# Kernel optimization log

Hardware: AMD Instinct MI355X
Metric: run time of the kernel (lower is better)

The kernel has to match this reference:

```python
import jax, jax.numpy as jnp
import numpy as np

TOP_K = 8
ROUTED_SCALING = 2.5


def setup_inputs() -> dict:
    key = jax.random.key(0)
    ks = jax.random.split(key, 8)
    B, S, H, E, I = 2, 1024, 2048, 32, 1024
    IS = 2 * I  # shared expert intermediate (n_shared_experts * moe_intermediate_size)
    w = lambda k, shape: jax.random.normal(k, shape, dtype=jnp.float32) * 0.02
    return {
        "hidden_states": jax.random.normal(ks[0], (B, S, H), dtype=jnp.float32),
        "gate_weight": w(ks[1], (E, H)),
        "w_gate": w(ks[2], (E, H, I)),
        "w_up": w(ks[3], (E, H, I)),
        "w_down": w(ks[4], (E, I, H)),
        "ws_gate": w(ks[5], (H, IS)),
        "ws_up": w(ks[6], (H, IS)),
        "ws_down": w(ks[7], (IS, H)),
    }


def reference(hidden_states, gate_weight, w_gate, w_up, w_down, ws_gate, ws_up, ws_down):
    B, S, H = hidden_states.shape
    x = hidden_states.reshape(-1, H)  # [T, H]
    T = x.shape[0]
    E = gate_weight.shape[0]

    # --- gate (DeepseekV3 top-k router: sigmoid scores, top-k, renormalize, scale) ---
    scores = jax.nn.sigmoid(x @ gate_weight.T)              # [T, E]
    topk_w, topk_i = jax.lax.top_k(scores, TOP_K)           # [T, K]
    topk_w = topk_w / (jnp.sum(topk_w, axis=-1, keepdims=True) + 1e-20)
    topk_w = topk_w * ROUTED_SCALING

    # dense [T, E] combine weights (scatter of top-k weights; zeros elsewhere)
    dense_w = jnp.zeros((T, E), dtype=topk_w.dtype).at[
        jnp.arange(T)[:, None], topk_i
    ].add(topk_w)

    # --- all experts on all tokens (calibrate_all_experts semantics; non-selected get weight 0) ---
    g = jnp.einsum('th,ehi->eti', x, w_gate)                # [E, T, I]
    u = jnp.einsum('th,ehi->eti', x, w_up)                  # [E, T, I]
    eo = jnp.einsum('eti,eih->eth', jax.nn.silu(g) * u, w_down)  # [E, T, H]
    routed = jnp.einsum('eth,te->th', eo, dense_w)          # weighted scatter-combine

    # --- shared expert (gated SiLU MLP on residual) ---
    shared = (jax.nn.silu(x @ ws_gate) * (x @ ws_up)) @ ws_down

    return (routed + shared).reshape(B, S, H)
```

## Files before the change

kernel.cpp:

```cpp
#include <hip/hip_runtime.h>

#define T_TOK 2048
#define H_DIM 2048
#define E_NUM 32
#define I_DIM 1024
#define IS_DIM 2048
#define K_TOT (E_NUM * I_DIM + IS_DIM)
#define SLOT_CAP 2048
#define MAX_TILES 160

typedef __bf16 bf16x8 __attribute__((ext_vector_type(8)));
typedef float  f32x4  __attribute__((ext_vector_type(4)));
static_assert(sizeof(bf16x8) == 16, "bf16x8 must be 16B");

#define OFF_CNT   ((size_t)0)
#define OFF_NT    ((size_t)128)
#define OFF_TILES ((size_t)256)
#define OFF_PAIRS ((size_t)1024)
#define OFF_XB    ((size_t)263168)
#define OFF_WGT   ((size_t)8651776)
#define OFF_WUT   ((size_t)142869504)
#define OFF_HS    OFF_WUT
#define OFF_WSGT  ((size_t)277087232)
#define OFF_WSUT  ((size_t)285475840)
#define OFF_WDT   ((size_t)293864448)
#define OFF_ACT   ((size_t)436470784)

__device__ __forceinline__ unsigned short f2bf(float f) {
  unsigned int u = __float_as_uint(f);
  u += 0x7fffu + ((u >> 16) & 1u);
  return (unsigned short)(u >> 16);
}

__device__ __forceinline__ void gld16(const void* g, void* l) {
  __builtin_amdgcn_global_load_lds(
      (const __attribute__((address_space(1))) unsigned int*)g,
      (__attribute__((address_space(3))) unsigned int*)l, 16, 0, 0);
}

__global__ __launch_bounds__(256) void router_kernel(
    const float* __restrict__ x, const float* __restrict__ gw,
    int* __restrict__ cnt, unsigned int* __restrict__ pairs)
{
  const int t = blockIdx.x;
  __shared__ float xs[H_DIM];
  __shared__ float sc[E_NUM];
  const float4* xr = (const float4*)(x + (long)t * H_DIM);
  for (int i = threadIdx.x; i < H_DIM / 4; i += 256) ((float4*)xs)[i] = xr[i];
  __syncthreads();
  const int e = threadIdx.x >> 3, p = threadIdx.x & 7;
  const float4* ga = (const float4*)(gw + (long)e * H_DIM);
  const float4* xa = (const float4*)xs;
  float s = 0.f;
  #pragma unroll 4
  for (int i = p * 64; i < p * 64 + 64; ++i) {
    float4 a = ga[i], b = xa[i];
    s += a.x * b.x + a.y * b.y + a.z * b.z + a.w * b.w;
  }
  s += __shfl_down(s, 4, 8);
  s += __shfl_down(s, 2, 8);
  s += __shfl_down(s, 1, 8);
  if (p == 0) sc[e] = 1.f / (1.f + expf(-s));
  __syncthreads();
  if (threadIdx.x == 0) {
    float v[E_NUM];
    #pragma unroll
    for (int i = 0; i < E_NUM; ++i) v[i] = sc[i];
    unsigned mask = 0; float sum = 0.f;
    int sel[8]; float wv[8];
    for (int k = 0; k < 8; ++k) {
      float best = -1.f; int bi = 0;
      for (int i = 0; i < E_NUM; ++i)
        if (!((mask >> i) & 1u) && v[i] > best) { best = v[i]; bi = i; }
      mask |= 1u << bi; sel[k] = bi; wv[k] = best; sum += best;
    }
    const float scale = 2.5f / (sum + 1e-20f);
    for (int k = 0; k < 8; ++k) {
      const int slot = atomicAdd(&cnt[sel[k]], 1);
      if (slot < SLOT_CAP) {
        const unsigned int w16 = (unsigned int)f2bf(wv[k] * scale);
        pairs[sel[k] * SLOT_CAP + slot] = (w16 << 16) | (unsigned int)t;
      }
    }
  }
}

__global__ void build_tiles_kernel(const int* __restrict__ cnt,
                                   unsigned int* __restrict__ tiles,
                                   int* __restrict__ ntp)
{
  if (threadIdx.x == 0 && blockIdx.x == 0) {
    int n = 0;
    for (int e = 0; e < E_NUM; ++e) {
      const int c = cnt[e];
      for (int m0 = 0; m0 < c; m0 += 128)
        tiles[n++] = ((unsigned int)e << 16) | (unsigned int)m0;
    }
    *ntp = n;
  }
}

__global__ __launch_bounds__(256) void cvt_bf16_kernel(
    const float* __restrict__ in, unsigned short* __restrict__ out, int n4)
{
  int i = blockIdx.x * 256 + threadIdx.x;
  if (i >= n4) return;
  float4 v = ((const float4*)in)[i];
  ushort4 o;
  o.x = f2bf(v.x); o.y = f2bf(v.y); o.z = f2bf(v.z); o.w = f2bf(v.w);
  ((ushort4*)out)[i] = o;
}

struct TDescTable {
  const float* in[6];
  unsigned short* out[6];
  int C[6];
  int ldout[6];
  long in_bs[6];
  long out_bs[6];
  int nbx[6];
  int nbxy[6];
  int start[7];
};

__global__ __launch_bounds__(256) void transpose_fused(TDescTable td)
{
  const int bid = blockIdx.x;
  int i = 0;
  while (i < 5 && bid >= td.start[i + 1]) ++i;
  const int local = bid - td.start[i];
  const int bz = local / td.nbxy[i];
  const int rem = local % td.nbxy[i];
  const int by = rem / td.nbx[i];
  const int bx = rem % td.nbx[i];
  const float* in = td.in[i] + (long)bz * td.in_bs[i];
  unsigned short* out = td.out[i] + (long)bz * td.out_bs[i];
  const int C = td.C[i], ldout = td.ldout[i];

  __shared__ float tile[64][65];
  const int c0 = bx * 64;
  const int r0 = by * 64;
  const int t = threadIdx.x;
  const int lr = t >> 4;
  const int lc = (t & 15) << 2;
  #pragma unroll
  for (int rr = 0; rr < 64; rr += 16) {
    float4 v = *(const float4*)(in + (long)(r0 + lr + rr) * C + c0 + lc);
    tile[lr + rr][lc + 0] = v.x;
    tile[lr + rr][lc + 1] = v.y;
    tile[lr + rr][lc + 2] = v.z;
    tile[lr + rr][lc + 3] = v.w;
  }
  __syncthreads();
  #pragma unroll
  for (int rr = 0; rr < 64; rr += 16) {
    const int c = c0 + lr + rr;
    ushort4 o;
    o.x = f2bf(tile[lc + 0][lr + rr]);
    o.y = f2bf(tile[lc + 1][lr + rr]);
    o.z = f2bf(tile[lc + 2][lr + rr]);
    o.w = f2bf(tile[lc + 3][lr + rr]);
    *(ushort4*)(out + (long)c * ldout + r0 + lc) = o;
  }
}

__global__ __launch_bounds__(512, 4) void gate_up_moe_kernel(
    const unsigned short* __restrict__ xb,
    const unsigned short* __restrict__ bgT,
    const unsigned short* __restrict__ buT,
    const int* __restrict__ cnt,
    const unsigned int* __restrict__ pairs,
    const unsigned int* __restrict__ tiles,
    const int* __restrict__ ntp,
    unsigned short* __restrict__ act)
{
  const int ti = blockIdx.y;
  if (ti >= *ntp) return;
  const unsigned int tile = tiles[ti];
  const int e  = (int)(tile >> 16);
  const int m0 = (int)(tile & 0xFFFFu);
  const int cnte = cnt[e];
  const int n0 = blockIdx.x * 64;
  const unsigned short* Bg = bgT + ((long)e * I_DIM + n0) * H_DIM;
  const unsigned short* Bu = buT + ((long)e * I_DIM + n0) * H_DIM;

  __shared__ unsigned short sA[2][128 * 64];
  __shared__ unsigned short sBg[2][64 * 64];
  __shared__ unsigned short sBu[2][64 * 64];

  const int tid = threadIdx.x;
  const int lane = tid & 63;
  const int wid = tid >> 6;
  const int wm = wid >> 1, wn = wid & 1;
  const int l15 = lane & 15;
  const int lk  = (lane >> 4) * 8;
  const int srow = tid >> 3;
  const int scol = (tid & 7) * 8;
  const int scolsw = (((tid & 7) ^ (srow & 7))) * 8;
  const int ksw = (l15 & 7) << 3;

  const unsigned short* asrc[2];
  #pragma unroll
  for (int r = 0; r < 2; ++r) {
    const int slot = m0 + r * 64 + srow;
    const unsigned int pr = (slot < cnte) ? pairs[e * SLOT_CAP + slot] : 0u;
    asrc[r] = xb + (long)(pr & 0xFFFFu) * H_DIM + scolsw;
  }

  const f32x4 fz = {0.f, 0.f, 0.f, 0.f};
  f32x4 accg[2][2], accu[2][2];
  #pragma unroll
  for (int i = 0; i < 2; ++i)
    #pragma unroll
    for (int j = 0; j < 2; ++j) { accg[i][j] = fz; accu[i][j] = fz; }

#define STAGE_GU(buf, k0) do {                                                 \
    gld16(asrc[0] + (k0), sA[buf] + srow * 64 + scol);                         \
    gld16(asrc[1] + (k0), sA[buf] + (64 + srow) * 64 + scol);                  \
    gld16(Bg + (long)srow * H_DIM + (k0) + scolsw,                             \
          sBg[buf] + srow * 64 + scol);                                        \
    gld16(Bu + (long)srow * H_DIM + (k0) + scolsw,                             \
          sBu[buf] + srow * 64 + scol);                                        \
  } while (0)

#define COMP_GU(buf) do {                                                      \
    _Pragma("unroll")                                                          \
    for (int kk = 0; kk < 2; ++kk) {                                           \
      const int ko = kk * 32 + lk;                                             \
      bf16x8 a[2], g[2], u[2];                                                 \
      _Pragma("unroll")                                                        \
      for (int mi = 0; mi < 2; ++mi)                                           \
        a[mi] = *(const bf16x8*)(sA[buf] + (wm * 32 + mi * 16 + l15) * 64 +    \
                                 (ko ^ ksw));                                  \
      _Pragma("unroll")                                                        \
      for (int ni = 0; ni < 2; ++ni) {                                         \
        g[ni] = *(const bf16x8*)(sBg[buf] + (wn * 32 + ni * 16 + l15) * 64 +   \
                                 (ko ^ ksw));                                  \
        u[ni] = *(const bf16x8*)(sBu[buf] + (wn * 32 + ni * 16 + l15) * 64 +   \
                                 (ko ^ ksw));                                  \
      }                                                                        \
      _Pragma("unroll")                                                        \
      for (int mi = 0; mi < 2; ++mi)                                           \
        _Pragma("unroll")                                                      \
        for (int ni = 0; ni < 2; ++ni) {                                       \
          accg[mi][ni] = __builtin_amdgcn_mfma_f32_16x16x32_bf16(              \
              a[mi], g[ni], accg[mi][ni], 0, 0, 0);                            \
          accu[mi][ni] = __builtin_amdgcn_mfma_f32_16x16x32_bf16(              \
              a[mi], u[ni], accu[mi][ni], 0, 0, 0);                            \
        }                                                                      \
    }                                                                          \
  } while (0)

  STAGE_GU(0, 0);
  __syncthreads();
  for (int t = 0; t < 32; t += 2) {
    if (t + 1 < 32) STAGE_GU(1, (t + 1) * 64);
    COMP_GU(0);
    __syncthreads();
    if (t + 2 < 32) STAGE_GU(0, (t + 2) * 64);
    COMP_GU(1);
    __syncthreads();
  }
#undef STAGE_GU
#undef COMP_GU

  const int colb = n0 + wn * 32;
  #pragma unroll
  for (int mi = 0; mi < 2; ++mi) {
    #pragma unroll
    for (int r = 0; r < 4; ++r) {
      const int slot = m0 + wm * 32 + mi * 16 + (lane >> 4) * 4 + r;
      if (slot < cnte) {
        const unsigned int pr = pairs[e * SLOT_CAP + slot];
        const float w = __uint_as_float(pr & 0xFFFF0000u);
        #pragma unroll
        for (int ni = 0; ni < 2; ++ni) {
          const float gv = accg[mi][ni][r];
          const float uv = accu[mi][ni][r];
          const float sv = (gv / (1.f + expf(-gv))) * uv * w;
          act[((long)e * SLOT_CAP + slot) * I_DIM + colb + ni * 16 + l15] =
              f2bf(sv);
        }
      }
    }
  }
}

__global__ __launch_bounds__(256) void gate_up_shared_kernel(
    const unsigned short* __restrict__ xb,
    const unsigned short* __restrict__ bgT,
    const unsigned short* __restrict__ buT,
    unsigned short* __restrict__ hs)
{
  const int t0 = blockIdx.x * 128;
  const int n0 = blockIdx.y * 64;
  const unsigned short* Bg = bgT + (long)n0 * H_DIM;
  const unsigned short* Bu = buT + (long)n0 * H_DIM;
  const unsigned short* A  = xb + (long)t0 * H_DIM;

  __shared__ unsigned short sA[128 * 64];
  __shared__ unsigned short sBg[64 * 64];
  __shared__ unsigned short sBu[64 * 64];

  const int tid = threadIdx.x;
  const int lane = tid & 63;
  const int wid = tid >> 6;
  const int wm = wid >> 1, wn = wid & 1;
  const int l15 = lane & 15;
  const int lk  = (lane >> 4) * 8;
  const int srow = tid >> 3;
  const int scol = (tid & 7) * 8;
  const int scolsw = (((tid & 7) ^ ((tid >> 3) & 7))) * 8;
  const int ksw = (l15 & 7) << 3;

  const f32x4 fz = {0.f, 0.f, 0.f, 0.f};
  f32x4 accg[4][2], accu[4][2];
  #pragma unroll
  for (int i = 0; i < 4; ++i)
    #pragma unroll
    for (int j = 0; j < 2; ++j) { accg[i][j] = fz; accu[i][j] = fz; }

  for (int k0 = 0; k0 < H_DIM; k0 += 64) {
    #pragma unroll
    for (int r = 0; r < 4; ++r)
      gld16(A + (long)(r * 32 + srow) * H_DIM + k0 + scolsw,
            sA + (r * 32 + srow) * 64 + scol);
    #pragma unroll
    for (int r = 0; r < 2; ++r) {
      gld16(Bg + (long)(r * 32 + srow) * H_DIM + k0 + scolsw,
            sBg + (r * 32 + srow) * 64 + scol);
      gld16(Bu + (long)(r * 32 + srow) * H_DIM + k0 + scolsw,
            sBu + (r * 32 + srow) * 64 + scol);
    }
    __syncthreads();
    #pragma unroll
    for (int kk = 0; kk < 2; ++kk) {
      const int ko = kk * 32 + lk;
      bf16x8 a[4], g[2], u[2];
      #pragma unroll
      for (int mi = 0; mi < 4; ++mi)
        a[mi] = *(const bf16x8*)(sA + (wm * 64 + mi * 16 + l15) * 64 + (ko ^ ksw));
      #pragma unroll
      for (int ni = 0; ni < 2; ++ni) {
        g[ni] = *(const bf16x8*)(sBg + (wn * 32 + ni * 16 + l15) * 64 + (ko ^ ksw));
        u[ni] = *(const bf16x8*)(sBu + (wn * 32 + ni * 16 + l15) * 64 + (ko ^ ksw));
      }
      #pragma unroll
      for (int mi = 0; mi < 4; ++mi)
        #pragma unroll
        for (int ni = 0; ni < 2; ++ni) {
          accg[mi][ni] = __builtin_amdgcn_mfma_f32_16x16x32_bf16(a[mi], g[ni], accg[mi][ni], 0, 0, 0);
          accu[mi][ni] = __builtin_amdgcn_mfma_f32_16x16x32_bf16(a[mi], u[ni], accu[mi][ni], 0, 0, 0);
        }
    }
    __syncthreads();
  }

  const int colb = n0 + wn * 32;
  #pragma unroll
  for (int mi = 0; mi < 4; ++mi) {
    #pragma unroll
    for (int r = 0; r < 4; ++r) {
      const int t = t0 + wm * 64 + mi * 16 + (lane >> 4) * 4 + r;
      #pragma unroll
      for (int ni = 0; ni < 2; ++ni) {
        const float gv = accg[mi][ni][r];
        const float uv = accu[mi][ni][r];
        hs[(long)t * IS_DIM + colb + ni * 16 + l15] =
            f2bf((gv / (1.f + expf(-gv))) * uv);
      }
    }
  }
}

__global__ __launch_bounds__(256) void down_shared_kernel(
    const unsigned short* __restrict__ hs,
    const unsigned short* __restrict__ wdT,
    float* __restrict__ out)
{
  const int t0 = blockIdx.x * 128;
  const int n0 = blockIdx.y * 64;
  const unsigned short* A = hs + (long)t0 * IS_DIM;
  const unsigned short* B = wdT + (long)n0 * K_TOT;

  __shared__ unsigned short sA[128 * 64];
  __shared__ unsigned short sB[64 * 64];

  const int tid = threadIdx.x;
  const int lane = tid & 63;
  const int wid = tid >> 6;
  const int wm = wid >> 1, wn = wid & 1;
  const int l15 = lane & 15;
  const int lk  = (lane >> 4) * 8;
  const int srow = tid >> 3;
  const int scol = (tid & 7) * 8;
  const int scolsw = (((tid & 7) ^ ((tid >> 3) & 7))) * 8;
  const int ksw = (l15 & 7) << 3;

  const f32x4 fz = {0.f, 0.f, 0.f, 0.f};
  f32x4 acc[4][2];
  #pragma unroll
  for (int i = 0; i < 4; ++i)
    #pragma unroll
    for (int j = 0; j < 2; ++j) acc[i][j] = fz;

  for (int k0 = 0; k0 < IS_DIM; k0 += 64) {
    #pragma unroll
    for (int r = 0; r < 4; ++r)
      gld16(A + (long)(r * 32 + srow) * IS_DIM + k0 + scolsw,
            sA + (r * 32 + srow) * 64 + scol);
    #pragma unroll
    for (int r = 0; r < 2; ++r)
      gld16(B + (long)(r * 32 + srow) * K_TOT + k0 + scolsw,
            sB + (r * 32 + srow) * 64 + scol);
    __syncthreads();
    #pragma unroll
    for (int kk = 0; kk < 2; ++kk) {
      const int ko = kk * 32 + lk;
      bf16x8 a[4], b[2];
      #pragma unroll
      for (int mi = 0; mi < 4; ++mi)
        a[mi] = *(const bf16x8*)(sA + (wm * 64 + mi * 16 + l15) * 64 + (ko ^ ksw));
      #pragma unroll
      for (int ni = 0; ni < 2; ++ni)
        b[ni] = *(const bf16x8*)(sB + (wn * 32 + ni * 16 + l15) * 64 + (ko ^ ksw));
      #pragma unroll
      for (int mi = 0; mi < 4; ++mi)
        #pragma unroll
        for (int ni = 0; ni < 2; ++ni)
          acc[mi][ni] = __builtin_amdgcn_mfma_f32_16x16x32_bf16(a[mi], b[ni], acc[mi][ni], 0, 0, 0);
    }
    __syncthreads();
  }

  #pragma unroll
  for (int mi = 0; mi < 4; ++mi) {
    #pragma unroll
    for (int r = 0; r < 4; ++r) {
      const int t = t0 + wm * 64 + mi * 16 + (lane >> 4) * 4 + r;
      #pragma unroll
      for (int ni = 0; ni < 2; ++ni)
        out[(long)t * H_DIM + n0 + wn * 32 + ni * 16 + l15] = acc[mi][ni][r];
    }
  }
}

__global__ __launch_bounds__(512, 4) void down_moe_kernel(
    const unsigned short* __restrict__ act,
    const unsigned short* __restrict__ wdT,
    const int* __restrict__ cnt,
    const unsigned int* __restrict__ pairs,
    const unsigned int* __restrict__ tiles,
    const int* __restrict__ ntp,
    float* __restrict__ out)
{
  const int ti = blockIdx.y;
  if (ti >= *ntp) return;
  const unsigned int tile = tiles[ti];
  const int e  = (int)(tile >> 16);
  const int m0 = (int)(tile & 0xFFFFu);
  const int cnte = cnt[e];
  const int n0 = blockIdx.x * 64;
  const unsigned short* A = act + ((long)e * SLOT_CAP + m0) * I_DIM;
  const unsigned short* B = wdT + (long)n0 * K_TOT + (long)e * I_DIM;

  __shared__ unsigned short sA[2][128 * 64];
  __shared__ unsigned short sB[2][64 * 64];

  const int tid = threadIdx.x;
  const int lane = tid & 63;
  const int wid = tid >> 6;
  const int wm = wid >> 1, wn = wid & 1;
  const int l15 = lane & 15;
  const int lk  = (lane >> 4) * 8;
  const int srow = tid >> 3;
  const int scol = (tid & 7) * 8;
  const int scolsw = (((tid & 7) ^ (srow & 7))) * 8;
  const int ksw = (l15 & 7) << 3;

  const f32x4 fz = {0.f, 0.f, 0.f, 0.f};
  f32x4 acc[2][2];
  #pragma unroll
  for (int i = 0; i < 2; ++i)
    #pragma unroll
    for (int j = 0; j < 2; ++j) acc[i][j] = fz;

#define STAGE_DN(buf, k0) do {                                                 \
    gld16(A + (long)srow * I_DIM + (k0) + scolsw,                              \
          sA[buf] + srow * 64 + scol);                                         \
    gld16(A + (long)(64 + srow) * I_DIM + (k0) + scolsw,                       \
          sA[buf] + (64 + srow) * 64 + scol);                                  \
    gld16(B + (long)srow * K_TOT + (k0) + scolsw,                              \
          sB[buf] + srow * 64 + scol);                                         \
  } while (0)

#define COMP_DN(buf) do {                                                      \
    _Pragma("unroll")                                                          \
    for (int kk = 0; kk < 2; ++kk) {                                           \
      const int ko = kk * 32 + lk;                                             \
      bf16x8 a[2], b[2];                                                       \
      _Pragma("unroll")                                                        \
      for (int mi = 0; mi < 2; ++mi)                                           \
        a[mi] = *(const bf16x8*)(sA[buf] + (wm * 32 + mi * 16 + l15) * 64 +    \
                                 (ko ^ ksw));                                  \
      _Pragma("unroll")                                                        \
      for (int ni = 0; ni < 2; ++ni)                                           \
        b[ni] = *(const bf16x8*)(sB[buf] + (wn * 32 + ni * 16 + l15) * 64 +    \
                                 (ko ^ ksw));                                  \
      _Pragma("unroll")                                                        \
      for (int mi = 0; mi < 2; ++mi)                                           \
        _Pragma("unroll")                                                      \
        for (int ni = 0; ni < 2; ++ni)                                         \
          acc[mi][ni] = __builtin_amdgcn_mfma_f32_16x16x32_bf16(               \
              a[mi], b[ni], acc[mi][ni], 0, 0, 0);                             \
    }                                                                          \
  } while (0)

  STAGE_DN(0, 0);
  __syncthreads();
  for (int t = 0; t < 16; t += 2) {
    if (t + 1 < 16) STAGE_DN(1, (t + 1) * 64);
    COMP_DN(0);
    __syncthreads();
    if (t + 2 < 16) STAGE_DN(0, (t + 2) * 64);
    COMP_DN(1);
    __syncthreads();
  }
#undef STAGE_DN
#undef COMP_DN

  #pragma unroll
  for (int mi = 0; mi < 2; ++mi) {
    #pragma unroll
    for (int r = 0; r < 4; ++r) {
      const int slot = m0 + wm * 32 + mi * 16 + (lane >> 4) * 4 + r;
      if (slot < cnte) {
        const int tok = (int)(pairs[e * SLOT_CAP + slot] & 0xFFFFu);
        #pragma unroll
        for (int ni = 0; ni < 2; ++ni)
          atomicAdd(out + (long)tok * H_DIM + n0 + wn * 32 + ni * 16 + l15,
                    acc[mi][ni][r]);
      }
    }
  }
}

extern "C" void kernel_launch(void* const* d_in, const int* in_sizes, int n_in,
                              void* d_out, int out_size, void* d_ws, size_t ws_size,
                              hipStream_t stream) {
  (void)in_sizes; (void)n_in; (void)out_size; (void)ws_size;
  const float* x   = (const float*)d_in[0];
  const float* gw  = (const float*)d_in[1];
  const float* wg  = (const float*)d_in[2];
  const float* wu  = (const float*)d_in[3];
  const float* wd  = (const float*)d_in[4];
  const float* wsg = (const float*)d_in[5];
  const float* wsu = (const float*)d_in[6];
  const float* wsd = (const float*)d_in[7];
  float* out = (float*)d_out;
  char* ws = (char*)d_ws;

  int*            cnt   = (int*)(ws + OFF_CNT);
  int*            ntp   = (int*)(ws + OFF_NT);
  unsigned int*   tiles = (unsigned int*)(ws + OFF_TILES);
  unsigned int*   pairs = (unsigned int*)(ws + OFF_PAIRS);
  unsigned short* xb    = (unsigned short*)(ws + OFF_XB);
  unsigned short* wgT   = (unsigned short*)(ws + OFF_WGT);
  unsigned short* wuT   = (unsigned short*)(ws + OFF_WUT);
  unsigned short* hsb   = (unsigned short*)(ws + OFF_HS);
  unsigned short* wsgT  = (unsigned short*)(ws + OFF_WSGT);
  unsigned short* wsuT  = (unsigned short*)(ws + OFF_WSUT);
  unsigned short* wdT   = (unsigned short*)(ws + OFF_WDT);
  unsigned short* actb  = (unsigned short*)(ws + OFF_ACT);

  hipMemsetAsync(ws + OFF_CNT, 0, 128, stream);

  router_kernel<<<T_TOK, 256, 0, stream>>>(x, gw, cnt, pairs);
  build_tiles_kernel<<<1, 64, 0, stream>>>(cnt, tiles, ntp);
  cvt_bf16_kernel<<<(T_TOK * H_DIM / 4 + 255) / 256, 256, 0, stream>>>(
      x, xb, T_TOK * H_DIM / 4);

  TDescTable td;
  td.in[0] = wg;  td.out[0] = wgT;  td.C[0] = I_DIM;  td.ldout[0] = H_DIM;
  td.in_bs[0] = (long)H_DIM * I_DIM; td.out_bs[0] = (long)I_DIM * H_DIM;
  td.nbx[0] = I_DIM / 64; td.nbxy[0] = (I_DIM / 64) * (H_DIM / 64);
  td.in[1] = wu;  td.out[1] = wuT;  td.C[1] = I_DIM;  td.ldout[1] = H_DIM;
  td.in_bs[1] = (long)H_DIM * I_DIM; td.out_bs[1] = (long)I_DIM * H_DIM;
  td.nbx[1] = I_DIM / 64; td.nbxy[1] = (I_DIM / 64) * (H_DIM / 64);
  td.in[2] = wd;  td.out[2] = wdT;  td.C[2] = H_DIM;  td.ldout[2] = K_TOT;
  td.in_bs[2] = (long)I_DIM * H_DIM; td.out_bs[2] = (long)I_DIM;
  td.nbx[2] = H_DIM / 64; td.nbxy[2] = (H_DIM / 64) * (I_DIM / 64);
  td.in[3] = wsg; td.out[3] = wsgT; td.C[3] = IS_DIM; td.ldout[3] = H_DIM;
  td.in_bs[3] = 0; td.out_bs[3] = 0;
  td.nbx[3] = IS_DIM / 64; td.nbxy[3] = (IS_DIM / 64) * (H_DIM / 64);
  td.in[4] = wsu; td.out[4] = wsuT; td.C[4] = IS_DIM; td.ldout[4] = H_DIM;
  td.in_bs[4] = 0; td.out_bs[4] = 0;
  td.nbx[4] = IS_DIM / 64; td.nbxy[4] = (IS_DIM / 64) * (H_DIM / 64);
  td.in[5] = wsd; td.out[5] = wdT + E_NUM * I_DIM; td.C[5] = H_DIM;
  td.ldout[5] = K_TOT; td.in_bs[5] = 0; td.out_bs[5] = 0;
  td.nbx[5] = H_DIM / 64; td.nbxy[5] = (H_DIM / 64) * (IS_DIM / 64);
  td.start[0] = 0;
  for (int i = 0; i < 5; ++i) {
    int nz = (i <= 2) ? E_NUM : 1;
    td.start[i + 1] = td.start[i] + td.nbxy[i] * nz;
  }
  td.start[6] = td.start[5] + td.nbxy[5];
  transpose_fused<<<td.start[6], 256, 0, stream>>>(td);

  gate_up_moe_kernel<<<dim3(16, MAX_TILES), 512, 0, stream>>>(
      xb, wgT, wuT, cnt, pairs, tiles, ntp, actb);

  gate_up_shared_kernel<<<dim3(16, 32), 256, 0, stream>>>(
      xb, wsgT, wsuT, hsb);

  down_shared_kernel<<<dim3(16, 32), 256, 0, stream>>>(
      hsb, wdT + E_NUM * I_DIM, out);
  down_moe_kernel<<<dim3(32, MAX_TILES), 512, 0, stream>>>(
      actb, wdT, cnt, pairs, tiles, ntp, out);
}
```

Measured before the change: 865.8 us.

## Fold shared expert into grouped MoE GEMMs as pseudo-experts; widen transpose tiles

The shared expert is treated as two extra pseudo-experts (32, 33) with all tokens and weight 1.0. This lets the grouped gate/up and down kernels handle it, and the two separate shared-expert kernels are removed. Activations are packed compactly using per-expert base offsets. The down kernel runs 32 K-steps for the shared tile, with address remapping across the two halves. The transpose kernel now converts to bf16 before writing to LDS and uses 64x256 tiles with 16-byte stores. The output must be zeroed with a memset because everything now accumulates atomically, which adds atomic traffic for the shared part.

```diff
diff --git a/kernel.cpp b/kernel.cpp
--- a/kernel.cpp
+++ b/kernel.cpp
@@ -7,24 +7,29 @@
 #define IS_DIM 2048
 #define K_TOT (E_NUM * I_DIM + IS_DIM)
 #define SLOT_CAP 2048
-#define MAX_TILES 160
+#define NE_ALL 34
+#define GU_TILES 192
+#define DN_TILES 176
+#define ACT_SLOTS 24576
 
 typedef __bf16 bf16x8 __attribute__((ext_vector_type(8)));
 typedef float  f32x4  __attribute__((ext_vector_type(4)));
 static_assert(sizeof(bf16x8) == 16, "bf16x8 must be 16B");
 
 #define OFF_CNT   ((size_t)0)
-#define OFF_NT    ((size_t)128)
-#define OFF_TILES ((size_t)256)
-#define OFF_PAIRS ((size_t)1024)
-#define OFF_XB    ((size_t)263168)
-#define OFF_WGT   ((size_t)8651776)
-#define OFF_WUT   ((size_t)142869504)
-#define OFF_HS    OFF_WUT
-#define OFF_WSGT  ((size_t)277087232)
-#define OFF_WSUT  ((size_t)285475840)
-#define OFF_WDT   ((size_t)293864448)
-#define OFF_ACT   ((size_t)436470784)
+#define OFF_NTGU  ((size_t)192)
+#define OFF_NTDN  ((size_t)196)
+#define OFF_BASE  ((size_t)256)
+#define OFF_TGU   ((size_t)512)
+#define OFF_TDN   ((size_t)1280)
+#define OFF_PAIRS ((size_t)2048)
+#define OFF_XB    ((size_t)280576)
+#define OFF_WGT   ((size_t)8669184)
+#define OFF_WUT   ((size_t)142886912)
+#define OFF_WSGT  ((size_t)277104640)
+#define OFF_WSUT  ((size_t)285493248)
+#define OFF_WDT   ((size_t)293881856)
+#define OFF_ACT   ((size_t)436488192)
 
 __device__ __forceinline__ unsigned short f2bf(float f) {
   unsigned int u = __float_as_uint(f);
@@ -85,18 +90,31 @@
   }
 }
 
-__global__ void build_tiles_kernel(const int* __restrict__ cnt,
-                                   unsigned int* __restrict__ tiles,
-                                   int* __restrict__ ntp)
-{
-  if (threadIdx.x == 0 && blockIdx.x == 0) {
-    int n = 0;
-    for (int e = 0; e < E_NUM; ++e) {
-      const int c = cnt[e];
-      for (int m0 = 0; m0 < c; m0 += 128)
-        tiles[n++] = ((unsigned int)e << 16) | (unsigned int)m0;
+__global__ __launch_bounds__(256) void build_tiles_kernel(
+    int* __restrict__ cnt, int* __restrict__ base,
+    unsigned int* __restrict__ tgu, int* __restrict__ ntgu,
+    unsigned int* __restrict__ tdn, int* __restrict__ ntdn,
+    unsigned int* __restrict__ pairs)
+{
+  const int t = threadIdx.x;
+  for (int s = t; s < T_TOK; s += 256) {
+    const unsigned int pv = (0x3F80u << 16) | (unsigned int)s;
+    pairs[32 * SLOT_CAP + s] = pv;
+    pairs[33 * SLOT_CAP + s] = pv;
+  }
+  if (t == 0) {
+    cnt[32] = T_TOK; cnt[33] = T_TOK;
+    int b = 0, ngu = 0, ndn = 0;
+    for (int e = 0; e < NE_ALL; ++e) {
+      const int c = (e < 32) ? cnt[e] : T_TOK;
+      base[e] = b;
+      for (int m0 = 0; m0 < c; m0 += 128) {
+        tgu[ngu++] = ((unsigned int)e << 16) | (unsigned int)m0;
+        if (e < 33) tdn[ndn++] = ((unsigned int)e << 16) | (unsigned int)m0;
+      }
+      b += (c + 127) & ~127;
     }
-    *ntp = n;
+    *ntgu = ngu; *ntdn = ndn;
   }
 }
 
@@ -137,30 +155,34 @@
   unsigned short* out = td.out[i] + (long)bz * td.out_bs[i];
   const int C = td.C[i], ldout = td.ldout[i];
 
-  __shared__ float tile[64][65];
+  __shared__ unsigned short tile[64][258];
   const int c0 = bx * 64;
-  const int r0 = by * 64;
+  const int r0 = by * 256;
   const int t = threadIdx.x;
-  const int lr = t >> 4;
-  const int lc = (t & 15) << 2;
-  #pragma unroll
-  for (int rr = 0; rr < 64; rr += 16) {
-    float4 v = *(const float4*)(in + (long)(r0 + lr + rr) * C + c0 + lc);
-    tile[lr + rr][lc + 0] = v.x;
-    tile[lr + rr][lc + 1] = v.y;
-    tile[lr + rr][lc + 2] = v.z;
-    tile[lr + rr][lc + 3] = v.w;
+  const int rl0 = t >> 4;
+  const int cl0 = (t & 15) * 4;
+  #pragma unroll
+  for (int p = 0; p < 16; ++p) {
+    const int rl = p * 16 + rl0;
+    float4 v = *(const float4*)(in + (long)(r0 + rl) * C + c0 + cl0);
+    tile[cl0 + 0][rl] = f2bf(v.x);
+    tile[cl0 + 1][rl] = f2bf(v.y);
+    tile[cl0 + 2][rl] = f2bf(v.z);
+    tile[cl0 + 3][rl] = f2bf(v.w);
   }
   __syncthreads();
-  #pragma unroll
-  for (int rr = 0; rr < 64; rr += 16) {
-    const int c = c0 + lr + rr;
-    ushort4 o;
-    o.x = f2bf(tile[lc + 0][lr + rr]);
-    o.y = f2bf(tile[lc + 1][lr + rr]);
-    o.z = f2bf(tile[lc + 2][lr + rr]);
-    o.w = f2bf(tile[lc + 3][lr + rr]);
-    *(ushort4*)(out + (long)c * ldout + r0 + lc) = o;
+  const int cw = t >> 5;
+  const int rw = (t & 31) * 8;
+  #pragma unroll
+  for (int q = 0; q < 8; ++q) {
+    const int cl = q * 8 + cw;
+    const char* src = (const char*)&tile[cl][rw];
+    uint4 o;
+    o.x = *(const unsigned int*)(src + 0);
+    o.y = *(const unsigned int*)(src + 4);
+    o.z = *(const unsigned int*)(src + 8);
+    o.w = *(const unsigned int*)(src + 12);
+    *(uint4*)(out + (long)(c0 + cl) * ldout + r0 + rw) = o;
   }
 }
 
@@ -168,7 +190,10 @@
     const unsigned short* __restrict__ xb,
     const unsigned short* __restrict__ bgT,
     const unsigned short* __restrict__ buT,
+    const unsigned short* __restrict__ sgT,
+    const unsigned short* __restrict__ suT,
     const int* __restrict__ cnt,
+    const int* __restrict__ base,
     const unsigned int* __restrict__ pairs,
     const unsigned int* __restrict__ tiles,
     const int* __restrict__ ntp,
@@ -180,9 +205,13 @@
   const int e  = (int)(tile >> 16);
   const int m0 = (int)(tile & 0xFFFFu);
   const int cnte = cnt[e];
+  const int be = base[e];
   const int n0 = blockIdx.x * 64;
-  const unsigned short* Bg = bgT + ((long)e * I_DIM + n0) * H_DIM;
-  const unsigned short* Bu = buT + ((long)e * I_DIM + n0) * H_DIM;
+  const long panel = (long)I_DIM * H_DIM;
+  const unsigned short* Bg =
+      ((e < 32) ? bgT + e * panel : sgT + (e - 32) * panel) + (long)n0 * H_DIM;
+  const unsigned short* Bu =
+      ((e < 32) ? buT + e * panel : suT + (e - 32) * panel) + (long)n0 * H_DIM;
 
   __shared__ unsigned short sA[2][128 * 64];
   __shared__ unsigned short sBg[2][64 * 64];
@@ -278,169 +307,9 @@
           const float gv = accg[mi][ni][r];
           const float uv = accu[mi][ni][r];
           const float sv = (gv / (1.f + expf(-gv))) * uv * w;
-          act[((long)e * SLOT_CAP + slot) * I_DIM + colb + ni * 16 + l15] =
-              f2bf(sv);
+          act[((long)(be + slot)) * I_DIM + colb + ni * 16 + l15] = f2bf(sv);
         }
       }
-    }
-  }
-}
-
-__global__ __launch_bounds__(256) void gate_up_shared_kernel(
-    const unsigned short* __restrict__ xb,
-    const unsigned short* __restrict__ bgT,
-    const unsigned short* __restrict__ buT,
-    unsigned short* __restrict__ hs)
-{
-  const int t0 = blockIdx.x * 128;
-  const int n0 = blockIdx.y * 64;
-  const unsigned short* Bg = bgT + (long)n0 * H_DIM;
-  const unsigned short* Bu = buT + (long)n0 * H_DIM;
-  const unsigned short* A  = xb + (long)t0 * H_DIM;
-
-  __shared__ unsigned short sA[128 * 64];
-  __shared__ unsigned short sBg[64 * 64];
-  __shared__ unsigned short sBu[64 * 64];
-
-  const int tid = threadIdx.x;
-  const int lane = tid & 63;
-  const int wid = tid >> 6;
-  const int wm = wid >> 1, wn = wid & 1;
-  const int l15 = lane & 15;
-  const int lk  = (lane >> 4) * 8;
-  const int srow = tid >> 3;
-  const int scol = (tid & 7) * 8;
-  const int scolsw = (((tid & 7) ^ ((tid >> 3) & 7))) * 8;
-  const int ksw = (l15 & 7) << 3;
-
-  const f32x4 fz = {0.f, 0.f, 0.f, 0.f};
-  f32x4 accg[4][2], accu[4][2];
-  #pragma unroll
-  for (int i = 0; i < 4; ++i)
-    #pragma unroll
-    for (int j = 0; j < 2; ++j) { accg[i][j] = fz; accu[i][j] = fz; }
-
-  for (int k0 = 0; k0 < H_DIM; k0 += 64) {
-    #pragma unroll
-    for (int r = 0; r < 4; ++r)
-      gld16(A + (long)(r * 32 + srow) * H_DIM + k0 + scolsw,
-            sA + (r * 32 + srow) * 64 + scol);
-    #pragma unroll
-    for (int r = 0; r < 2; ++r) {
-      gld16(Bg + (long)(r * 32 + srow) * H_DIM + k0 + scolsw,
-            sBg + (r * 32 + srow) * 64 + scol);
-      gld16(Bu + (long)(r * 32 + srow) * H_DIM + k0 + scolsw,
-            sBu + (r * 32 + srow) * 64 + scol);
-    }
-    __syncthreads();
-    #pragma unroll
-    for (int kk = 0; kk < 2; ++kk) {
-      const int ko = kk * 32 + lk;
-      bf16x8 a[4], g[2], u[2];
-      #pragma unroll
-      for (int mi = 0; mi < 4; ++mi)
-        a[mi] = *(const bf16x8*)(sA + (wm * 64 + mi * 16 + l15) * 64 + (ko ^ ksw));
-      #pragma unroll
-      for (int ni = 0; ni < 2; ++ni) {
-        g[ni] = *(const bf16x8*)(sBg + (wn * 32 + ni * 16 + l15) * 64 + (ko ^ ksw));
-        u[ni] = *(const bf16x8*)(sBu + (wn * 32 + ni * 16 + l15) * 64 + (ko ^ ksw));
-      }
-      #pragma unroll
-      for (int mi = 0; mi < 4; ++mi)
-        #pragma unroll
-        for (int ni = 0; ni < 2; ++ni) {
-          accg[mi][ni] = __builtin_amdgcn_mfma_f32_16x16x32_bf16(a[mi], g[ni], accg[mi][ni], 0, 0, 0);
-          accu[mi][ni] = __builtin_amdgcn_mfma_f32_16x16x32_bf16(a[mi], u[ni], accu[mi][ni], 0, 0, 0);
-        }
-    }
-    __syncthreads();
-  }
-
-  const int colb = n0 + wn * 32;
-  #pragma unroll
-  for (int mi = 0; mi < 4; ++mi) {
-    #pragma unroll
-    for (int r = 0; r < 4; ++r) {
-      const int t = t0 + wm * 64 + mi * 16 + (lane >> 4) * 4 + r;
-      #pragma unroll
-      for (int ni = 0; ni < 2; ++ni) {
-        const float gv = accg[mi][ni][r];
-        const float uv = accu[mi][ni][r];
-        hs[(long)t * IS_DIM + colb + ni * 16 + l15] =
-            f2bf((gv / (1.f + expf(-gv))) * uv);
-      }
-    }
-  }
-}
-
-__global__ __launch_bounds__(256) void down_shared_kernel(
-    const unsigned short* __restrict__ hs,
-    const unsigned short* __restrict__ wdT,
-    float* __restrict__ out)
-{
-  const int t0 = blockIdx.x * 128;
-  const int n0 = blockIdx.y * 64;
-  const unsigned short* A = hs + (long)t0 * IS_DIM;
-  const unsigned short* B = wdT + (long)n0 * K_TOT;
-
-  __shared__ unsigned short sA[128 * 64];
-  __shared__ unsigned short sB[64 * 64];
-
-  const int tid = threadIdx.x;
-  const int lane = tid & 63;
-  const int wid = tid >> 6;
-  const int wm = wid >> 1, wn = wid & 1;
-  const int l15 = lane & 15;
-  const int lk  = (lane >> 4) * 8;
-  const int srow = tid >> 3;
-  const int scol = (tid & 7) * 8;
-  const int scolsw = (((tid & 7) ^ ((tid >> 3) & 7))) * 8;
-  const int ksw = (l15 & 7) << 3;
-
-  const f32x4 fz = {0.f, 0.f, 0.f, 0.f};
-  f32x4 acc[4][2];
-  #pragma unroll
-  for (int i = 0; i < 4; ++i)
-    #pragma unroll
-    for (int j = 0; j < 2; ++j) acc[i][j] = fz;
-
-  for (int k0 = 0; k0 < IS_DIM; k0 += 64) {
-    #pragma unroll
-    for (int r = 0; r < 4; ++r)
-      gld16(A + (long)(r * 32 + srow) * IS_DIM + k0 + scolsw,
-            sA + (r * 32 + srow) * 64 + scol);
-    #pragma unroll
-    for (int r = 0; r < 2; ++r)
-      gld16(B + (long)(r * 32 + srow) * K_TOT + k0 + scolsw,
-            sB + (r * 32 + srow) * 64 + scol);
-    __syncthreads();
-    #pragma unroll
-    for (int kk = 0; kk < 2; ++kk) {
-      const int ko = kk * 32 + lk;
-      bf16x8 a[4], b[2];
-      #pragma unroll
-      for (int mi = 0; mi < 4; ++mi)
-        a[mi] = *(const bf16x8*)(sA + (wm * 64 + mi * 16 + l15) * 64 + (ko ^ ksw));
-      #pragma unroll
-      for (int ni = 0; ni < 2; ++ni)
-        b[ni] = *(const bf16x8*)(sB + (wn * 32 + ni * 16 + l15) * 64 + (ko ^ ksw));
-      #pragma unroll
-      for (int mi = 0; mi < 4; ++mi)
-        #pragma unroll
-        for (int ni = 0; ni < 2; ++ni)
-          acc[mi][ni] = __builtin_amdgcn_mfma_f32_16x16x32_bf16(a[mi], b[ni], acc[mi][ni], 0, 0, 0);
-    }
-    __syncthreads();
-  }
-
-  #pragma unroll
-  for (int mi = 0; mi < 4; ++mi) {
-    #pragma unroll
-    for (int r = 0; r < 4; ++r) {
-      const int t = t0 + wm * 64 + mi * 16 + (lane >> 4) * 4 + r;
-      #pragma unroll
-      for (int ni = 0; ni < 2; ++ni)
-        out[(long)t * H_DIM + n0 + wn * 32 + ni * 16 + l15] = acc[mi][ni][r];
     }
   }
 }
@@ -449,6 +318,7 @@
     const unsigned short* __restrict__ act,
     const unsigned short* __restrict__ wdT,
     const int* __restrict__ cnt,
+    const int* __restrict__ base,
     const unsigned int* __restrict__ pairs,
     const unsigned int* __restrict__ tiles,
     const int* __restrict__ ntp,
@@ -461,8 +331,9 @@
   const int m0 = (int)(tile & 0xFFFFu);
   const int cnte = cnt[e];
   const int n0 = blockIdx.x * 64;
-  const unsigned short* A = act + ((long)e * SLOT_CAP + m0) * I_DIM;
+  const unsigned short* A = act + ((long)base[e] + m0) * I_DIM;
   const unsigned short* B = wdT + (long)n0 * K_TOT + (long)e * I_DIM;
+  const int nk = (e == 32) ? 32 : 16;
 
   __shared__ unsigned short sA[2][128 * 64];
   __shared__ unsigned short sB[2][64 * 64];
@@ -486,9 +357,11 @@
     for (int j = 0; j < 2; ++j) acc[i][j] = fz;
 
 #define STAGE_DN(buf, k0) do {                                                 \
-    gld16(A + (long)srow * I_DIM + (k0) + scolsw,                              \
+    const long koff = (long)((k0) & 1023) +                                    \
+                      (long)((k0) >> 10) * (2048L * 1024L);                    \
+    gld16(A + (long)srow * I_DIM + koff + scolsw,                              \
           sA[buf] + srow * 64 + scol);                                         \
-    gld16(A + (long)(64 + srow) * I_DIM + (k0) + scolsw,                       \
+    gld16(A + (long)(64 + srow) * I_DIM + koff + scolsw,                       \
           sA[buf] + (64 + srow) * 64 + scol);                                  \
     gld16(B + (long)srow * K_TOT + (k0) + scolsw,                              \
           sB[buf] + srow * 64 + scol);                                         \
@@ -518,11 +391,11 @@
 
   STAGE_DN(0, 0);
   __syncthreads();
-  for (int t = 0; t < 16; t += 2) {
-    if (t + 1 < 16) STAGE_DN(1, (t + 1) * 64);
+  for (int t = 0; t < nk; t += 2) {
+    if (t + 1 < nk) STAGE_DN(1, (t + 1) * 64);
     COMP_DN(0);
     __syncthreads();
-    if (t + 2 < 16) STAGE_DN(0, (t + 2) * 64);
+    if (t + 2 < nk) STAGE_DN(0, (t + 2) * 64);
     COMP_DN(1);
     __syncthreads();
   }
@@ -548,7 +421,7 @@
 extern "C" void kernel_launch(void* const* d_in, const int* in_sizes, int n_in,
                               void* d_out, int out_size, void* d_ws, size_t ws_size,
                               hipStream_t stream) {
-  (void)in_sizes; (void)n_in; (void)out_size; (void)ws_size;
+  (void)in_sizes; (void)n_in; (void)ws_size;
   const float* x   = (const float*)d_in[0];
   const float* gw  = (const float*)d_in[1];
   const float* wg  = (const float*)d_in[2];
@@ -561,44 +434,48 @@
   char* ws = (char*)d_ws;
 
   int*            cnt   = (int*)(ws + OFF_CNT);
-  int*            ntp   = (int*)(ws + OFF_NT);
-  unsigned int*   tiles = (unsigned int*)(ws + OFF_TILES);
+  int*            ntgu  = (int*)(ws + OFF_NTGU);
+  int*            ntdn  = (int*)(ws + OFF_NTDN);
+  int*            basep = (int*)(ws + OFF_BASE);
+  unsigned int*   tgu   = (unsigned int*)(ws + OFF_TGU);
+  unsigned int*   tdn   = (unsigned int*)(ws + OFF_TDN);
   unsigned int*   pairs = (unsigned int*)(ws + OFF_PAIRS);
   unsigned short* xb    = (unsigned short*)(ws + OFF_XB);
   unsigned short* wgT   = (unsigned short*)(ws + OFF_WGT);
   unsigned short* wuT   = (unsigned short*)(ws + OFF_WUT);
-  unsigned short* hsb   = (unsigned short*)(ws + OFF_HS);
   unsigned short* wsgT  = (unsigned short*)(ws + OFF_WSGT);
   unsigned short* wsuT  = (unsigned short*)(ws + OFF_WSUT);
   unsigned short* wdT   = (unsigned short*)(ws + OFF_WDT);
   unsigned short* actb  = (unsigned short*)(ws + OFF_ACT);
 
-  hipMemsetAsync(ws + OFF_CNT, 0, 128, stream);
+  hipMemsetAsync(ws + OFF_CNT, 0, 256, stream);
+  hipMemsetAsync(out, 0, (size_t)out_size * sizeof(float), stream);
 
   router_kernel<<<T_TOK, 256, 0, stream>>>(x, gw, cnt, pairs);
-  build_tiles_kernel<<<1, 64, 0, stream>>>(cnt, tiles, ntp);
+  build_tiles_kernel<<<1, 256, 0, stream>>>(cnt, basep, tgu, ntgu, tdn, ntdn,
+                                            pairs);
   cvt_bf16_kernel<<<(T_TOK * H_DIM / 4 + 255) / 256, 256, 0, stream>>>(
       x, xb, T_TOK * H_DIM / 4);
 
   TDescTable td;
   td.in[0] = wg;  td.out[0] = wgT;  td.C[0] = I_DIM;  td.ldout[0] = H_DIM;
   td.in_bs[0] = (long)H_DIM * I_DIM; td.out_bs[0] = (long)I_DIM * H_DIM;
-  td.nbx[0] = I_DIM / 64; td.nbxy[0] = (I_DIM / 64) * (H_DIM / 64);
+  td.nbx[0] = I_DIM / 64; td.nbxy[0] = (I_DIM / 64) * (H_DIM / 256);
   td.in[1] = wu;  td.out[1] = wuT;  td.C[1] = I_DIM;  td.ldout[1] = H_DIM;
   td.in_bs[1] = (long)H_DIM * I_DIM; td.out_bs[1] = (long)I_DIM * H_DIM;
-  td.nbx[1] = I_DIM / 64; td.nbxy[1] = (I_DIM / 64) * (H_DIM / 64);
+  td.nbx[1] = I_DIM / 64; td.nbxy[1] = (I_DIM / 64) * (H_DIM / 256);
   td.in[2] = wd;  td.out[2] = wdT;  td.C[2] = H_DIM;  td.ldout[2] = K_TOT;
   td.in_bs[2] = (long)I_DIM * H_DIM; td.out_bs[2] = (long)I_DIM;
-  td.nbx[2] = H_DIM / 64; td.nbxy[2] = (H_DIM / 64) * (I_DIM / 64);
+  td.nbx[2] = H_DIM / 64; td.nbxy[2] = (H_DIM / 64) * (I_DIM / 256);
   td.in[3] = wsg; td.out[3] = wsgT; td.C[3] = IS_DIM; td.ldout[3] = H_DIM;
   td.in_bs[3] = 0; td.out_bs[3] = 0;
-  td.nbx[3] = IS_DIM / 64; td.nbxy[3] = (IS_DIM / 64) * (H_DIM / 64);
+  td.nbx[3] = IS_DIM / 64; td.nbxy[3] = (IS_DIM / 64) * (H_DIM / 256);
   td.in[4] = wsu; td.out[4] = wsuT; td.C[4] = IS_DIM; td.ldout[4] = H_DIM;
   td.in_bs[4] = 0; td.out_bs[4] = 0;
-  td.nbx[4] = IS_DIM / 64; td.nbxy[4] = (IS_DIM / 64) * (H_DIM / 64);
+  td.nbx[4] = IS_DIM / 64; td.nbxy[4] = (IS_DIM / 64) * (H_DIM / 256);
   td.in[5] = wsd; td.out[5] = wdT + E_NUM * I_DIM; td.C[5] = H_DIM;
   td.ldout[5] = K_TOT; td.in_bs[5] = 0; td.out_bs[5] = 0;
-  td.nbx[5] = H_DIM / 64; td.nbxy[5] = (H_DIM / 64) * (IS_DIM / 64);
+  td.nbx[5] = H_DIM / 64; td.nbxy[5] = (H_DIM / 64) * (IS_DIM / 256);
   td.start[0] = 0;
   for (int i = 0; i < 5; ++i) {
     int nz = (i <= 2) ? E_NUM : 1;
@@ -607,14 +484,9 @@
   td.start[6] = td.start[5] + td.nbxy[5];
   transpose_fused<<<td.start[6], 256, 0, stream>>>(td);
 
-  gate_up_moe_kernel<<<dim3(16, MAX_TILES), 512, 0, stream>>>(
-      xb, wgT, wuT, cnt, pairs, tiles, ntp, actb);
-
-  gate_up_shared_kernel<<<dim3(16, 32), 256, 0, stream>>>(
-      xb, wsgT, wsuT, hsb);
-
-  down_shared_kernel<<<dim3(16, 32), 256, 0, stream>>>(
-      hsb, wdT + E_NUM * I_DIM, out);
-  down_moe_kernel<<<dim3(32, MAX_TILES), 512, 0, stream>>>(
-      actb, wdT, cnt, pairs, tiles, ntp, out);
-}
+  gate_up_moe_kernel<<<dim3(16, GU_TILES), 512, 0, stream>>>(
+      xb, wgT, wuT, wsgT, wsuT, cnt, basep, pairs, tgu, ntgu, actb);
+
+  down_moe_kernel<<<dim3(32, DN_TILES), 512, 0, stream>>>(
+      actb, wdT, cnt, basep, pairs, tdn, ntdn, out);
+}
```

Result: no change. 860.9 us (-0.6%).
